# Kernel tuning notes

Measured on AMD Instinct MI355X. Metric: run time of the kernel, lower is better.

The kernel has to match this reference:

```python
import jax, jax.numpy as jnp
import numpy as np

NEG_SLOPE = 0.2
BN_EPS = 1e-5


def _gat(x, src, dst, W, a_src, a_dst, b, concat):
    """PyG GATConv (eval mode, self-loops already in src/dst)."""
    N = x.shape[0]
    H, C = a_src.shape
    h = (x @ W).reshape(N, H, C)                      # [N,H,C]
    s = (h * a_src).sum(-1)                           # [N,H] per-node src score
    d = (h * a_dst).sum(-1)                           # [N,H] per-node dst score
    e = jax.nn.leaky_relu(s[src] + d[dst], NEG_SLOPE)  # [E,H]
    m = jax.ops.segment_max(e, dst, num_segments=N)   # segment softmax over dst
    ex = jnp.exp(e - m[dst])
    denom = jax.ops.segment_sum(ex, dst, num_segments=N)
    alpha = ex / denom[dst]                           # [E,H]
    out = jax.ops.segment_sum(alpha[:, :, None] * h[src], dst, num_segments=N)  # [N,H,C]
    out = out.reshape(N, H * C) if concat else out.mean(axis=1)
    return out + b


def _bn(x, g, beta, rm, rv):
    return (x - rm) * (g / jnp.sqrt(rv + BN_EPS)) + beta


def setup_inputs() -> dict:
    key = jax.random.key(0)
    ks = jax.random.split(key, 32)
    N, E, IN, HID, H, NC = 50000, 400000, 768, 128, 4, 2
    d = {}
    d['x'] = jax.random.normal(ks[0], (N, IN), jnp.float32)
    d['edge_index'] = jax.random.randint(ks[1], (2, E), 0, N, jnp.int64)

    def lin(k, fan_in, shape):
        return jax.random.normal(k, shape, jnp.float32) * (1.0 / np.sqrt(fan_in))

    # layer 1: in=768 -> 4 heads x 128, concat
    d['W1'] = lin(ks[2], IN, (IN, H * HID)); d['a1s'] = lin(ks[3], HID, (H, HID))
    d['a1d'] = lin(ks[4], HID, (H, HID)); d['b1'] = jnp.zeros((H * HID,), jnp.float32)
    d['g1'] = jax.random.uniform(ks[5], (H * HID,), jnp.float32, 0.5, 1.5)
    d['be1'] = jax.random.normal(ks[6], (H * HID,), jnp.float32) * 0.1
    d['rm1'] = jax.random.normal(ks[7], (H * HID,), jnp.float32) * 0.1
    d['rv1'] = jax.random.uniform(ks[8], (H * HID,), jnp.float32, 0.5, 1.5)
    d['W2'] = lin(ks[9], H * HID, (H * HID, H * HID)); d['a2s'] = lin(ks[10], HID, (H, HID))
    d['a2d'] = lin(ks[11], HID, (H, HID)); d['b2'] = jnp.zeros((H * HID,), jnp.float32)
    d['g2'] = jax.random.uniform(ks[12], (H * HID,), jnp.float32, 0.5, 1.5)
    d['be2'] = jax.random.normal(ks[13], (H * HID,), jnp.float32) * 0.1
    d['rm2'] = jax.random.normal(ks[14], (H * HID,), jnp.float32) * 0.1
    d['rv2'] = jax.random.uniform(ks[15], (H * HID,), jnp.float32, 0.5, 1.5)
    # layer 3: 512 -> 1 head x 128, mean (concat=False)
    d['W3'] = lin(ks[16], H * HID, (H * HID, HID)); d['a3s'] = lin(ks[17], HID, (1, HID))
    d['a3d'] = lin(ks[18], HID, (1, HID)); d['b3'] = jnp.zeros((HID,), jnp.float32)
    d['g3'] = jax.random.uniform(ks[19], (HID,), jnp.float32, 0.5, 1.5)
    d['be3'] = jax.random.normal(ks[20], (HID,), jnp.float32) * 0.1
    d['rm3'] = jax.random.normal(ks[21], (HID,), jnp.float32) * 0.1
    d['rv3'] = jax.random.uniform(ks[22], (HID,), jnp.float32, 0.5, 1.5)
    # classifier 128 -> 2
    d['Wc'] = lin(ks[23], HID, (HID, NC)); d['bc'] = jnp.zeros((NC,), jnp.float32)
    return d


def reference(x, edge_index, W1, a1s, a1d, b1, g1, be1, rm1, rv1,
              W2, a2s, a2d, b2, g2, be2, rm2, rv2,
              W3, a3s, a3d, b3, g3, be3, rm3, rv3, Wc, bc):
    N = x.shape[0]
    loops = jnp.arange(N, dtype=edge_index.dtype)  # GATConv add_self_loops=True
    src = jnp.concatenate([edge_index[0], loops])
    dst = jnp.concatenate([edge_index[1], loops])

    h = _gat(x, src, dst, W1, a1s, a1d, b1, concat=True)
    h = jax.nn.elu(_bn(h, g1, be1, rm1, rv1))          # dropout: eval mode (identity)
    h = _gat(h, src, dst, W2, a2s, a2d, b2, concat=True)
    h = jax.nn.elu(_bn(h, g2, be2, rm2, rv2))
    h = _gat(h, src, dst, W3, a3s, a3d, b3, concat=False)
    h = jax.nn.elu(_bn(h, g3, be3, rm3, rv3))
    return h @ Wc + bc                                  # [N, 2] logits
```

## Files before the change

### kernel.cpp

```cpp
#include <hip/hip_runtime.h>
#include <hip/hip_bf16.h>
#include <math.h>

constexpr int IN_F = 768;
constexpr float NEG_SLOPE = 0.2f;
constexpr float BN_EPS = 1e-5f;

typedef __attribute__((ext_vector_type(8))) short short8;
typedef __attribute__((ext_vector_type(4))) float f32x4;

__device__ inline float bf2f(unsigned short u) {
    unsigned int x = ((unsigned int)u) << 16;
    return __uint_as_float(x);
}
__device__ inline unsigned short f2bf(float f) {
    __hip_bfloat16 h = __float2bfloat16(f);
    return *(unsigned short*)&h;
}
__device__ inline void gload_lds16(const unsigned short* g, unsigned short* l) {
    __builtin_amdgcn_global_load_lds(
        (const __attribute__((address_space(1))) void*)g,
        (__attribute__((address_space(3))) void*)l, 16, 0, 0);
}


__global__ void count_edges(const int* __restrict__ dst, int E, int* __restrict__ count) {
    int e = blockIdx.x * blockDim.x + threadIdx.x;
    if (e < E) atomicAdd(&count[dst[e]], 1);
}

__global__ void scan_counts(const int* __restrict__ count, int* __restrict__ row_start, int N) {
    __shared__ int wsum[17];
    __shared__ int carry;
    int tid = threadIdx.x;
    int lane = tid & 63, w = tid >> 6;
    if (tid == 0) carry = 0;
    __syncthreads();
    for (int base = 0; base < N; base += 16384) {
        int idx = base + tid * 16;
        int v[16];
        if (idx + 16 <= N) {
            #pragma unroll
            for (int j = 0; j < 4; j++) {
                int4 t4 = *(const int4*)&count[idx + j * 4];
                v[j * 4 + 0] = t4.x; v[j * 4 + 1] = t4.y;
                v[j * 4 + 2] = t4.z; v[j * 4 + 3] = t4.w;
            }
        } else {
            #pragma unroll
            for (int j = 0; j < 16; j++) v[j] = (idx + j < N) ? count[idx + j] : 0;
        }
        int tsum = 0;
        #pragma unroll
        for (int j = 0; j < 16; j++) tsum += v[j];
        int x = tsum;
        #pragma unroll
        for (int off = 1; off < 64; off <<= 1) {
            int y = __shfl_up(x, off, 64);
            if (lane >= off) x += y;
        }
        if (lane == 63) wsum[w] = x;
        __syncthreads();
        if (tid == 0) {
            int r = 0;
            for (int i = 0; i < 16; i++) { int t = wsum[i]; wsum[i] = r; r += t; }
            wsum[16] = r;
        }
        __syncthreads();
        int excl = carry + wsum[w] + (x - tsum);
        #pragma unroll
        for (int j = 0; j < 16; j++) {
            if (idx + j < N) row_start[idx + j] = excl;
            excl += v[j];
        }
        __syncthreads();
        if (tid == 0) carry += wsum[16];
        __syncthreads();
    }
    if (tid == 0) row_start[N] = carry;
}

__global__ void scatter_edges(const int* __restrict__ srcA, const int* __restrict__ dstA,
                              int E, int N, const int* __restrict__ row_start,
                              int* __restrict__ cursor, int* __restrict__ col) {
    int i = blockIdx.x * blockDim.x + threadIdx.x;
    if (i < E) {
        int d = dstA[i];
        int pos = row_start[d] + atomicAdd(&cursor[d], 1);
        col[pos] = srcA[i];
    } else if (i < E + N) {
        int n = i - E;
        int pos = row_start[n] + atomicAdd(&cursor[n], 1);
        col[pos] = n;
    }
}


__global__ void cast_w(const float* __restrict__ W1, const float* __restrict__ W2,
                       const float* __restrict__ W3, unsigned short* __restrict__ Wt1,
                       unsigned short* __restrict__ Wt2, unsigned short* __restrict__ Wt3,
                       int* __restrict__ count, int* __restrict__ cursor, int N) {
    int j = blockIdx.x * blockDim.x + threadIdx.x;
    const int S1 = 768 * 512, S2 = 512 * 512, S3 = 512 * 128;
    if (j < S1) {
        int k = j / 512, n = j % 512;
        Wt1[(size_t)n * 768 + k] = f2bf(W1[j]);
    } else if (j < S1 + S2) {
        int jj = j - S1;
        int k = jj / 512, n = jj % 512;
        Wt2[(size_t)n * 512 + k] = f2bf(W2[jj]);
    } else if (j < S1 + S2 + S3) {
        int jj = j - S1 - S2;
        int k = jj / 128, n = jj % 128;
        Wt3[(size_t)n * 512 + k] = f2bf(W3[jj]);
    } else {
        int j2 = j - (S1 + S2 + S3);
        if (j2 < N) { count[j2] = 1; cursor[j2] = 0; }
    }
}


template <bool CAST_A>
__global__ __launch_bounds__(256, 3) void gemm_bf16(const unsigned short* __restrict__ A,
                                                    const float* __restrict__ Af,
                                                    const unsigned short* __restrict__ Wt,
                                                    unsigned short* __restrict__ C,
                                                    const float* __restrict__ a_s,
                                                    const float* __restrict__ a_d,
                                                    float* __restrict__ s1,
                                                    float* __restrict__ d1,
                                                    int M, int Nc, int K, int H) {
    __shared__ __align__(16) unsigned short As[128 * 64];
    __shared__ __align__(16) unsigned short Bs[128 * 64];
    const int tid = threadIdx.x;
    const int lane = tid & 63;
    const int wave = tid >> 6;
    const int wm = wave >> 1, wn = wave & 1;

    const int l = blockIdx.x;
    const int x = l & 7;
    const int t0 = l >> 3;
    const int HT = Nc >> 7;
    const int by = (HT == 4) ? (t0 & 3) : 0;
    const int g  = (HT == 4) ? (t0 >> 2) : t0;
    const int rb = g * 8 + x;
    const int row0 = rb * 128, col0 = by * 128;
    if (row0 >= M) return;

    f32x4 acc[4][4];
    #pragma unroll
    for (int i = 0; i < 4; i++)
        #pragma unroll
        for (int j = 0; j < 4; j++)
            acc[i][j] = (f32x4){0.f, 0.f, 0.f, 0.f};

    const int ldm = tid >> 3;
    const int kpart = (((tid & 7) ^ ((tid >> 3) & 7)) * 8);
    const int fr = lane & 15;
    const int quad = lane >> 4;

    for (int k0 = 0; k0 < K; k0 += 64) {
        __syncthreads();
        if constexpr (CAST_A) {
            #pragma unroll
            for (int ih = 0; ih < 2; ih++) {
                float4 fa[2][2];
                #pragma unroll
                for (int i2 = 0; i2 < 2; i2++) {
                    int i = ih * 2 + i2;
                    int gr = row0 + i * 32 + ldm; if (gr >= M) gr = M - 1;
                    const float* src = Af + (size_t)gr * K + k0 + kpart;
                    fa[i2][0] = *(const float4*)src;
                    fa[i2][1] = *(const float4*)(src + 4);
                }
                #pragma unroll
                for (int i2 = 0; i2 < 2; i2++) {
                    int i = ih * 2 + i2;
                    uint4 p;
                    p.x = (unsigned int)f2bf(fa[i2][0].x) | ((unsigned int)f2bf(fa[i2][0].y) << 16);
                    p.y = (unsigned int)f2bf(fa[i2][0].z) | ((unsigned int)f2bf(fa[i2][0].w) << 16);
                    p.z = (unsigned int)f2bf(fa[i2][1].x) | ((unsigned int)f2bf(fa[i2][1].y) << 16);
                    p.w = (unsigned int)f2bf(fa[i2][1].z) | ((unsigned int)f2bf(fa[i2][1].w) << 16);
                    *(uint4*)&As[i * 2048 + tid * 8] = p;
                }
            }
            #pragma unroll
            for (int i = 0; i < 4; i++) {
                int n = col0 + i * 32 + ldm;
                gload_lds16(Wt + (size_t)n * K + k0 + kpart, &Bs[i * 2048 + tid * 8]);
            }
        } else {
            #pragma unroll
            for (int i = 0; i < 4; i++) {
                int gr = row0 + i * 32 + ldm; if (gr >= M) gr = M - 1;
                gload_lds16(A + (size_t)gr * K + k0 + kpart, &As[i * 2048 + tid * 8]);
                int n = col0 + i * 32 + ldm;
                gload_lds16(Wt + (size_t)n * K + k0 + kpart, &Bs[i * 2048 + tid * 8]);
            }
        }
        __syncthreads();
        #pragma unroll
        for (int s = 0; s < 2; s++) {
            const int slot8 = (((s << 2) + quad) ^ (fr & 7)) * 8;
            short8 a[4], b[4];
            #pragma unroll
            for (int tt = 0; tt < 4; tt++) {
                a[tt] = *(const short8*)&As[(wm * 64 + tt * 16 + fr) * 64 + slot8];
                b[tt] = *(const short8*)&Bs[(wn * 64 + tt * 16 + fr) * 64 + slot8];
            }
            #pragma unroll
            for (int mi = 0; mi < 4; mi++)
                #pragma unroll
                for (int ni = 0; ni < 4; ni++)
                    acc[mi][ni] = __builtin_amdgcn_mfma_f32_16x16x32_bf16(
                        a[mi], b[ni], acc[mi][ni], 0, 0, 0);
        }
    }

    const int rbase = row0 + wm * 64 + quad * 4;
    const int cbase = col0 + wn * 64 + fr;
    #pragma unroll
    for (int mi = 0; mi < 4; mi++) {
        #pragma unroll
        for (int reg = 0; reg < 4; reg++) {
            int r = rbase + mi * 16 + reg;
            if (r < M) {
                #pragma unroll
                for (int ni = 0; ni < 4; ni++)
                    C[(size_t)r * Nc + cbase + ni * 16] = f2bf(acc[mi][ni][reg]);
            }
        }
    }

    float asv[4], adv[4];
    #pragma unroll
    for (int ni = 0; ni < 4; ni++) {
        int c = by * 128 + wn * 64 + ni * 16 + fr;
        asv[ni] = a_s[c];
        adv[ni] = a_d[c];
    }
    float ps[4][4], pd[4][4];
    #pragma unroll
    for (int mi = 0; mi < 4; mi++)
        #pragma unroll
        for (int reg = 0; reg < 4; reg++) {
            float t = 0.f, u = 0.f;
            #pragma unroll
            for (int ni = 0; ni < 4; ni++) {
                t += acc[mi][ni][reg] * asv[ni];
                u += acc[mi][ni][reg] * adv[ni];
            }
            ps[mi][reg] = t;
            pd[mi][reg] = u;
        }
    #pragma unroll
    for (int off = 1; off <= 8; off <<= 1)
        #pragma unroll
        for (int mi = 0; mi < 4; mi++)
            #pragma unroll
            for (int reg = 0; reg < 4; reg++) {
                ps[mi][reg] += __shfl_xor(ps[mi][reg], off, 64);
                pd[mi][reg] += __shfl_xor(pd[mi][reg], off, 64);
            }
    float oS = 0.f, oD = 0.f;
    #pragma unroll
    for (int mi = 0; mi < 4; mi++)
        #pragma unroll
        for (int reg = 0; reg < 4; reg++)
            if (fr == mi * 4 + reg) { oS = ps[mi][reg]; oD = pd[mi][reg]; }
    int rw = rbase + (fr >> 2) * 16 + (fr & 3);

    __syncthreads();
    float* red = (float*)As;
    if (wn == 1) {
        red[wm * 64 + lane] = oS;
        red[128 + wm * 64 + lane] = oD;
    }
    __syncthreads();
    if (wn == 0) {
        float fS = oS + red[wm * 64 + lane];
        float fD = oD + red[128 + wm * 64 + lane];
        if (rw < M) {
            s1[(size_t)rw * H + by] = fS;
            d1[(size_t)rw * H + by] = fD;
        }
    }
}


__global__ void gat_agg_h4(const unsigned short* __restrict__ h,
                           const float* __restrict__ s1, const float* __restrict__ d1,
                           const int* __restrict__ row_start, const int* __restrict__ col,
                           const float* __restrict__ bias,
                           const float* __restrict__ gam, const float* __restrict__ beta,
                           const float* __restrict__ rm, const float* __restrict__ rv,
                           unsigned short* __restrict__ out, int N) {
    __shared__ float wlds[4][4][64];
    int lane = threadIdx.x & 63;
    int wid = threadIdx.x >> 6;
    int n = blockIdx.x * 4 + wid;
    if (n >= N) return;
    n = __builtin_amdgcn_readfirstlane(n);
    int beg = __builtin_amdgcn_readfirstlane(row_start[n]);
    int end = __builtin_amdgcn_readfirstlane(row_start[n + 1]);
    int hh = lane >> 4;
    unsigned ch0 = (unsigned)lane * 8;
    float4 dh4 = *(const float4*)&d1[(size_t)n * 4];

    float acc[8] = {0.f, 0.f, 0.f, 0.f, 0.f, 0.f, 0.f, 0.f};
    float denom = 0.f;

    for (int c0 = beg; c0 < end; c0 += 64) {
        int cnt = end - c0; if (cnt > 64) cnt = 64;
        int ce = c0 + (lane < cnt ? lane : cnt - 1);
        int cv = col[ce];
        float4 s4 = *(const float4*)&s1[(size_t)(unsigned)cv * 4];
        float live = (lane < cnt) ? 1.f : 0.f;
        float e0 = s4.x + dh4.x; e0 = e0 > 0.f ? e0 : NEG_SLOPE * e0;
        float e1 = s4.y + dh4.y; e1 = e1 > 0.f ? e1 : NEG_SLOPE * e1;
        float e2 = s4.z + dh4.z; e2 = e2 > 0.f ? e2 : NEG_SLOPE * e2;
        float e3 = s4.w + dh4.w; e3 = e3 > 0.f ? e3 : NEG_SLOPE * e3;
        wlds[wid][0][lane] = live * __expf(e0);
        wlds[wid][1][lane] = live * __expf(e1);
        wlds[wid][2][lane] = live * __expf(e2);
        wlds[wid][3][lane] = live * __expf(e3);

        int cend = c0 + cnt;
        for (int i = c0; i < cend; i += 8) {
            int base = i - c0;
            uint4 raw[8]; float w[8];
            #pragma unroll
            for (int u = 0; u < 8; u++) {
                int sn = __builtin_amdgcn_readlane(cv, base + u);
                w[u] = wlds[wid][hh][base + u];
                raw[u] = *(const uint4*)&h[((size_t)(unsigned)sn << 9) + ch0];
            }
            #pragma unroll
            for (int u = 0; u < 8; u++) {
                denom += w[u];
                acc[0] += w[u] * bf2f((unsigned short)(raw[u].x & 0xffff));
                acc[1] += w[u] * bf2f((unsigned short)(raw[u].x >> 16));
                acc[2] += w[u] * bf2f((unsigned short)(raw[u].y & 0xffff));
                acc[3] += w[u] * bf2f((unsigned short)(raw[u].y >> 16));
                acc[4] += w[u] * bf2f((unsigned short)(raw[u].z & 0xffff));
                acc[5] += w[u] * bf2f((unsigned short)(raw[u].z >> 16));
                acc[6] += w[u] * bf2f((unsigned short)(raw[u].w & 0xffff));
                acc[7] += w[u] * bf2f((unsigned short)(raw[u].w >> 16));
            }
        }
    }
    float inv = 1.f / denom;
    float v[8];
    #pragma unroll
    for (int c = 0; c < 8; c++) {
        int ch = ch0 + c;
        float t = acc[c] * inv + bias[ch];
        t = (t - rm[ch]) * (gam[ch] * rsqrtf(rv[ch] + BN_EPS)) + beta[ch];
        v[c] = t > 0.f ? t : expf(t) - 1.f;
    }
    uint4 p;
    p.x = (unsigned int)f2bf(v[0]) | ((unsigned int)f2bf(v[1]) << 16);
    p.y = (unsigned int)f2bf(v[2]) | ((unsigned int)f2bf(v[3]) << 16);
    p.z = (unsigned int)f2bf(v[4]) | ((unsigned int)f2bf(v[5]) << 16);
    p.w = (unsigned int)f2bf(v[6]) | ((unsigned int)f2bf(v[7]) << 16);
    *(uint4*)&out[((unsigned)n << 9) + ch0] = p;
}


__global__ void gat_agg_h1_cls(const unsigned short* __restrict__ h,
                               const float* __restrict__ s1, const float* __restrict__ d1,
                               const int* __restrict__ row_start, const int* __restrict__ col,
                               const float* __restrict__ bias,
                               const float* __restrict__ gam, const float* __restrict__ beta,
                               const float* __restrict__ rm, const float* __restrict__ rv,
                               const float* __restrict__ Wc, const float* __restrict__ bc,
                               float* __restrict__ out, int N) {
    int lane = threadIdx.x & 63;
    int wid = threadIdx.x >> 6;
    int n = blockIdx.x * 4 + wid;
    if (n >= N) return;
    n = __builtin_amdgcn_readfirstlane(n);
    int beg = __builtin_amdgcn_readfirstlane(row_start[n]);
    int end = __builtin_amdgcn_readfirstlane(row_start[n + 1]);
    int q = lane >> 4;
    int fl = lane & 15;
    const unsigned hoff = (unsigned)fl * 8;
    float dsum = d1[n];

    float acc[8] = {0.f, 0.f, 0.f, 0.f, 0.f, 0.f, 0.f, 0.f};
    float denom = 0.f;

    for (int c0 = beg; c0 < end; c0 += 64) {
        int cnt = end - c0; if (cnt > 64) cnt = 64;
        int ce = c0 + (lane < cnt ? lane : cnt - 1);
        int cv = col[ce];
        float ev = s1[(unsigned)cv] + dsum;
        ev = ev > 0.f ? ev : NEG_SLOPE * ev;
        float wv = (lane < cnt) ? __expf(ev) : 0.f;

        int cend = c0 + cnt;
        for (int i = c0; i < cend; i += 16) {
            int base = i - c0;
            uint4 raw[4]; float w[4];
            #pragma unroll
            for (int u = 0; u < 4; u++) {
                int urel = base + u * 4 + q;
                urel = urel < 63 ? urel : 63;
                int sn = __shfl(cv, urel, 64);
                w[u] = __shfl(wv, urel, 64);
                raw[u] = *(const uint4*)&h[((size_t)(unsigned)sn << 7) + hoff];
            }
            #pragma unroll
            for (int u = 0; u < 4; u++) {
                denom += w[u];
                acc[0] += w[u] * bf2f((unsigned short)(raw[u].x & 0xffff));
                acc[1] += w[u] * bf2f((unsigned short)(raw[u].x >> 16));
                acc[2] += w[u] * bf2f((unsigned short)(raw[u].y & 0xffff));
                acc[3] += w[u] * bf2f((unsigned short)(raw[u].y >> 16));
                acc[4] += w[u] * bf2f((unsigned short)(raw[u].z & 0xffff));
                acc[5] += w[u] * bf2f((unsigned short)(raw[u].z >> 16));
                acc[6] += w[u] * bf2f((unsigned short)(raw[u].w & 0xffff));
                acc[7] += w[u] * bf2f((unsigned short)(raw[u].w >> 16));
            }
        }
    }
    #pragma unroll
    for (int c = 0; c < 8; c++) {
        acc[c] += __shfl_xor(acc[c], 16, 64);
        acc[c] += __shfl_xor(acc[c], 32, 64);
    }
    denom += __shfl_xor(denom, 16, 64);
    denom += __shfl_xor(denom, 32, 64);

    if (q == 0) {
        float inv = 1.f / denom;
        int ch0 = fl * 8;
        float p0 = 0.f, p1 = 0.f;
        #pragma unroll
        for (int c = 0; c < 8; c++) {
            int ch = ch0 + c;
            float t = acc[c] * inv + bias[ch];
            t = (t - rm[ch]) * (gam[ch] * rsqrtf(rv[ch] + BN_EPS)) + beta[ch];
            t = t > 0.f ? t : expf(t) - 1.f;
            p0 += t * Wc[ch * 2 + 0];
            p1 += t * Wc[ch * 2 + 1];
        }
        #pragma unroll
        for (int off = 8; off >= 1; off >>= 1) {
            p0 += __shfl_xor(p0, off, 64);
            p1 += __shfl_xor(p1, off, 64);
        }
        if (fl == 0) {
            out[n * 2 + 0] = p0 + bc[0];
            out[n * 2 + 1] = p1 + bc[1];
        }
    }
}


extern "C" void kernel_launch(void* const* d_in, const int* in_sizes, int n_in,
                              void* d_out, int out_size, void* d_ws, size_t ws_size,
                              hipStream_t stream) {
    const float* x   = (const float*)d_in[0];
    const int*   ei  = (const int*)d_in[1];
    const float* W1  = (const float*)d_in[2];
    const float* a1s = (const float*)d_in[3];
    const float* a1d = (const float*)d_in[4];
    const float* b1  = (const float*)d_in[5];
    const float* gm1 = (const float*)d_in[6];
    const float* be1 = (const float*)d_in[7];
    const float* rm1 = (const float*)d_in[8];
    const float* rv1 = (const float*)d_in[9];
    const float* W2  = (const float*)d_in[10];
    const float* a2s = (const float*)d_in[11];
    const float* a2d = (const float*)d_in[12];
    const float* b2  = (const float*)d_in[13];
    const float* gm2 = (const float*)d_in[14];
    const float* be2 = (const float*)d_in[15];
    const float* rm2 = (const float*)d_in[16];
    const float* rv2 = (const float*)d_in[17];
    const float* W3  = (const float*)d_in[18];
    const float* a3s = (const float*)d_in[19];
    const float* a3d = (const float*)d_in[20];
    const float* b3  = (const float*)d_in[21];
    const float* gm3 = (const float*)d_in[22];
    const float* be3 = (const float*)d_in[23];
    const float* rm3 = (const float*)d_in[24];
    const float* rv3 = (const float*)d_in[25];
    const float* Wc  = (const float*)d_in[26];
    const float* bc  = (const float*)d_in[27];

    int N = in_sizes[0] / IN_F;
    int E = in_sizes[1] / 2;
    int P = E + N;
    const int* srcA = ei;
    const int* dstA = ei + E;

    unsigned short* hbuf = (unsigned short*)d_ws;
    unsigned short* gbuf = hbuf + (size_t)N * 512;
    float* s1   = (float*)(gbuf + (size_t)N * 512);
    float* d1   = s1 + (size_t)N * 4;
    unsigned short* Wt1 = (unsigned short*)(d1 + (size_t)N * 4);
    unsigned short* Wt2 = Wt1 + 512 * 768;
    unsigned short* Wt3 = Wt2 + 512 * 512;
    int* count     = (int*)(Wt3 + 128 * 512);
    int* cursor    = count + N;
    int* row_start = cursor + N;
    int* col       = row_start + N + 1;

    int ctot = 768 * 512 + 512 * 512 + 512 * 128 + N;
    cast_w<<<(ctot + 255) / 256, 256, 0, stream>>>(W1, W2, W3, Wt1, Wt2, Wt3,
                                                   count, cursor, N);
    count_edges<<<(E + 255) / 256, 256, 0, stream>>>(dstA, E, count);
    scan_counts<<<1, 1024, 0, stream>>>(count, row_start, N);
    scatter_edges<<<(E + N + 255) / 256, 256, 0, stream>>>(srcA, dstA, E, N, row_start,
                                                           cursor, col);

    int Mb = (N + 127) / 128;
    int MbP = (Mb + 7) & ~7;
    int Nb4 = (N + 3) / 4;

    gemm_bf16<true><<<4 * MbP, 256, 0, stream>>>(nullptr, x, Wt1, hbuf, a1s, a1d,
                                                 s1, d1, N, 512, 768, 4);
    gat_agg_h4<<<Nb4, 256, 0, stream>>>(hbuf, s1, d1, row_start, col,
                                        b1, gm1, be1, rm1, rv1, gbuf, N);
    gemm_bf16<false><<<4 * MbP, 256, 0, stream>>>(gbuf, nullptr, Wt2, hbuf, a2s, a2d,
                                                  s1, d1, N, 512, 512, 4);
    gat_agg_h4<<<Nb4, 256, 0, stream>>>(hbuf, s1, d1, row_start, col,
                                        b2, gm2, be2, rm2, rv2, gbuf, N);
    gemm_bf16<false><<<MbP, 256, 0, stream>>>(gbuf, nullptr, Wt3, hbuf, a3s, a3d,
                                              s1, d1, N, 128, 512, 1);
    gat_agg_h1_cls<<<Nb4, 256, 0, stream>>>(hbuf, s1, d1, row_start, col,
                                            b3, gm3, be3, rm3, rv3, Wc, bc, (float*)d_out, N);
}
```

Baseline: 640.5 us.

## Register-prefetch fp32 A tiles two steps ahead in cast GEMM path

In the fp32-input GEMM path (layer 1, K=768), the A tile loads are software-pipelined into two register buffers, so global reads for future k-steps are in flight while the MFMAs run on the current tile. Before, each k-step loaded fp32 A, converted it and wrote it to LDS synchronously before computing, which exposed global latency. This doubles the register footprint for staged A data (32 extra float4), which may reduce occupancy, and assumes K is a multiple of 128.

```diff
diff --git a/kernel.cpp b/kernel.cpp
--- a/kernel.cpp
+++ b/kernel.cpp
@@ -159,37 +159,76 @@
     const int fr = lane & 15;
     const int quad = lane >> 4;
 
-    for (int k0 = 0; k0 < K; k0 += 64) {
-        __syncthreads();
-        if constexpr (CAST_A) {
-            #pragma unroll
-            for (int ih = 0; ih < 2; ih++) {
-                float4 fa[2][2];
-                #pragma unroll
-                for (int i2 = 0; i2 < 2; i2++) {
-                    int i = ih * 2 + i2;
-                    int gr = row0 + i * 32 + ldm; if (gr >= M) gr = M - 1;
-                    const float* src = Af + (size_t)gr * K + k0 + kpart;
-                    fa[i2][0] = *(const float4*)src;
-                    fa[i2][1] = *(const float4*)(src + 4);
-                }
-                #pragma unroll
-                for (int i2 = 0; i2 < 2; i2++) {
-                    int i = ih * 2 + i2;
-                    uint4 p;
-                    p.x = (unsigned int)f2bf(fa[i2][0].x) | ((unsigned int)f2bf(fa[i2][0].y) << 16);
-                    p.y = (unsigned int)f2bf(fa[i2][0].z) | ((unsigned int)f2bf(fa[i2][0].w) << 16);
-                    p.z = (unsigned int)f2bf(fa[i2][1].x) | ((unsigned int)f2bf(fa[i2][1].y) << 16);
-                    p.w = (unsigned int)f2bf(fa[i2][1].z) | ((unsigned int)f2bf(fa[i2][1].w) << 16);
-                    *(uint4*)&As[i * 2048 + tid * 8] = p;
-                }
-            }
-            #pragma unroll
-            for (int i = 0; i < 4; i++) {
-                int n = col0 + i * 32 + ldm;
-                gload_lds16(Wt + (size_t)n * K + k0 + kpart, &Bs[i * 2048 + tid * 8]);
-            }
-        } else {
+    const float* arow[4];
+    if constexpr (CAST_A) {
+        #pragma unroll
+        for (int i = 0; i < 4; i++) {
+            int gr = row0 + i * 32 + ldm; if (gr >= M) gr = M - 1;
+            arow[i] = Af + (size_t)gr * K + kpart;
+        }
+    }
+
+    #define LOAD_FA(dst, off)                                    \
+        _Pragma("unroll")                                        \
+        for (int i = 0; i < 4; i++) {                            \
+            dst[i][0] = *(const float4*)(arow[i] + (off));       \
+            dst[i][1] = *(const float4*)(arow[i] + (off) + 4);   \
+        }
+    #define CVT_WRITE(src)                                                                  \
+        _Pragma("unroll")                                                                   \
+        for (int i = 0; i < 4; i++) {                                                       \
+            uint4 p;                                                                        \
+            p.x = (unsigned int)f2bf(src[i][0].x) | ((unsigned int)f2bf(src[i][0].y) << 16);\
+            p.y = (unsigned int)f2bf(src[i][0].z) | ((unsigned int)f2bf(src[i][0].w) << 16);\
+            p.z = (unsigned int)f2bf(src[i][1].x) | ((unsigned int)f2bf(src[i][1].y) << 16);\
+            p.w = (unsigned int)f2bf(src[i][1].z) | ((unsigned int)f2bf(src[i][1].w) << 16);\
+            *(uint4*)&As[i * 2048 + tid * 8] = p;                                           \
+        }
+    #define GLOAD_B(k0v)                                                          \
+        _Pragma("unroll")                                                         \
+        for (int i = 0; i < 4; i++) {                                             \
+            int n = col0 + i * 32 + ldm;                                          \
+            gload_lds16(Wt + (size_t)n * K + (k0v) + kpart, &Bs[i * 2048 + tid * 8]); \
+        }
+    #define MFMA_PHASE                                                                   \
+        _Pragma("unroll")                                                                \
+        for (int s = 0; s < 2; s++) {                                                    \
+            const int slot8 = (((s << 2) + quad) ^ (fr & 7)) * 8;                        \
+            short8 a[4], b[4];                                                           \
+            _Pragma("unroll")                                                            \
+            for (int tt = 0; tt < 4; tt++) {                                             \
+                a[tt] = *(const short8*)&As[(wm * 64 + tt * 16 + fr) * 64 + slot8];      \
+                b[tt] = *(const short8*)&Bs[(wn * 64 + tt * 16 + fr) * 64 + slot8];      \
+            }                                                                            \
+            _Pragma("unroll")                                                            \
+            for (int mi = 0; mi < 4; mi++)                                               \
+                _Pragma("unroll")                                                        \
+                for (int ni = 0; ni < 4; ni++)                                           \
+                    acc[mi][ni] = __builtin_amdgcn_mfma_f32_16x16x32_bf16(               \
+                        a[mi], b[ni], acc[mi][ni], 0, 0, 0);                             \
+        }
+
+    if constexpr (CAST_A) {
+        float4 fa0[4][2], fa1[4][2];
+        LOAD_FA(fa0, 0)
+        LOAD_FA(fa1, 64)
+        for (int k0 = 0; k0 < K; k0 += 128) {
+            __syncthreads();
+            GLOAD_B(k0)
+            CVT_WRITE(fa0)
+            __syncthreads();
+            if (k0 + 128 < K) { LOAD_FA(fa0, k0 + 128) }
+            MFMA_PHASE
+            __syncthreads();
+            GLOAD_B(k0 + 64)
+            CVT_WRITE(fa1)
+            __syncthreads();
+            if (k0 + 192 < K) { LOAD_FA(fa1, k0 + 192) }
+            MFMA_PHASE
+        }
+    } else {
+        for (int k0 = 0; k0 < K; k0 += 64) {
+            __syncthreads();
             #pragma unroll
             for (int i = 0; i < 4; i++) {
                 int gr = row0 + i * 32 + ldm; if (gr >= M) gr = M - 1;
@@ -197,25 +236,15 @@
                 int n = col0 + i * 32 + ldm;
                 gload_lds16(Wt + (size_t)n * K + k0 + kpart, &Bs[i * 2048 + tid * 8]);
             }
-        }
-        __syncthreads();
-        #pragma unroll
-        for (int s = 0; s < 2; s++) {
-            const int slot8 = (((s << 2) + quad) ^ (fr & 7)) * 8;
-            short8 a[4], b[4];
-            #pragma unroll
-            for (int tt = 0; tt < 4; tt++) {
-                a[tt] = *(const short8*)&As[(wm * 64 + tt * 16 + fr) * 64 + slot8];
-                b[tt] = *(const short8*)&Bs[(wn * 64 + tt * 16 + fr) * 64 + slot8];
-            }
-            #pragma unroll
-            for (int mi = 0; mi < 4; mi++)
-                #pragma unroll
-                for (int ni = 0; ni < 4; ni++)
-                    acc[mi][ni] = __builtin_amdgcn_mfma_f32_16x16x32_bf16(
-                        a[mi], b[ni], acc[mi][ni], 0, 0, 0);
-        }
-    }
+            __syncthreads();
+            MFMA_PHASE
+        }
+    }
+
+    #undef LOAD_FA
+    #undef CVT_WRITE
+    #undef GLOAD_B
+    #undef MFMA_PHASE
 
     const int rbase = row0 + wm * 64 + quad * 4;
     const int cbase = col0 + wn * 64 + fr;
```

New measurement: 871.1 us. +36.0%, slower.
